# Performance work log

Measured on AMD Instinct MI355X. Metric: run time of the kernel, lower is better.

The kernel has to match this reference:

```python
import jax, jax.numpy as jnp
import numpy as np

D_MODEL = 1024
NUM_HEADS = 16
D_K = D_MODEL // NUM_HEADS


def setup_inputs() -> dict:
    key = jax.random.key(0)
    ks = jax.random.split(key, 12)
    B, S, D = 2, 2048, D_MODEL
    s = 1.0 / np.sqrt(D)
    inp = {
        "Q": jax.random.normal(ks[0], (B, S, D), jnp.float32),
        "K": jax.random.normal(ks[1], (B, S, D), jnp.float32),
        "V": jax.random.normal(ks[2], (B, S, D), jnp.float32),
        "Wq": jax.random.normal(ks[3], (D, D), jnp.float32) * s,
        "bq": jax.random.normal(ks[4], (D,), jnp.float32) * s,
        "Wk": jax.random.normal(ks[5], (D, D), jnp.float32) * s,
        "bk": jax.random.normal(ks[6], (D,), jnp.float32) * s,
        "Wv": jax.random.normal(ks[7], (D, D), jnp.float32) * s,
        "bv": jax.random.normal(ks[8], (D,), jnp.float32) * s,
        "Wo": jax.random.normal(ks[9], (D, D), jnp.float32) * s,
        "bo": jax.random.normal(ks[10], (D,), jnp.float32) * s,
    }
    return inp


def _split_heads(x, B, S):
    # [B, S, D] -> [B, H, S, d_k]
    return x.reshape(B, S, NUM_HEADS, D_K).transpose(0, 2, 1, 3)


def reference(Q, K, V, Wq, bq, Wk, bk, Wv, bv, Wo, bo):
    B, S, D = Q.shape
    # torch nn.Linear: y = x @ W.T + b
    q = _split_heads(Q @ Wq.T + bq, B, S)
    k = _split_heads(K @ Wk.T + bk, B, S)
    v = _split_heads(V @ Wv.T + bv, B, S)
    scale = 1.0 / np.sqrt(D_K).astype(np.float32)
    # [B, H, S, S] attention scores (materialized, as in the original)
    scores = jnp.einsum('bhqd,bhkd->bhqk', q, k) * scale
    probs = jax.nn.softmax(scores, axis=-1)
    out = jnp.einsum('bhqk,bhkd->bhqd', probs, v)
    out = out.transpose(0, 2, 1, 3).reshape(B, S, D)
    return out @ Wo.T + bo
```

## Files before the change

### kernel.cpp

```cpp
#include <hip/hip_runtime.h>
#include <hip/hip_bf16.h>

#define S_LEN   2048
#define NHEADS  16
#define DKH     64
#define DMODEL  1024
#define NBATCH  2

typedef __bf16 bf16x8 __attribute__((ext_vector_type(8)));
typedef __bf16 bf16x4 __attribute__((ext_vector_type(4)));
typedef float  f32x4  __attribute__((ext_vector_type(4)));

typedef __attribute__((address_space(3))) void       lds_void;
typedef const __attribute__((address_space(1))) void glob_void;

__device__ __forceinline__ void glds16(const void* g, void* l) {
    __builtin_amdgcn_global_load_lds((glob_void*)g, (lds_void*)l, 16, 0, 0);
}

struct CvtArgs {
    const float* src[7];
    __bf16*      dst[7];
    int          n[7];
};

__global__ __launch_bounds__(256)
void cvt_all_k(CvtArgs a)
{
    const int t = blockIdx.y;
    const size_t i = ((size_t)blockIdx.x * 256 + threadIdx.x) * 8;
    if ((int)i >= a.n[t]) return;
    const float* s = a.src[t];
    f32x4 lo = *(const f32x4*)(s + i);
    f32x4 hi = *(const f32x4*)(s + i + 4);
    bf16x8 r;
#pragma unroll
    for (int k = 0; k < 4; ++k) { r[k] = (__bf16)lo[k]; r[4 + k] = (__bf16)hi[k]; }
    *(bf16x8*)(a.dst[t] + i) = r;
}

__device__ __forceinline__ void gemm_core(
    const __bf16* __restrict__ A, const __bf16* __restrict__ W,
    int m0, int n0, int K,
    __bf16 (*As)[32], __bf16 (*Ws)[32], f32x4 acc[4][4])
{
    const int tid  = threadIdx.x;
    const int lane = tid & 63;
    const int wv   = tid >> 6;
    const int l15  = lane & 15;
    const int quad = lane >> 4;
    const int wm   = wv >> 1;
    const int wn   = wv & 1;
    const int grow = lane >> 2;
    const int gcol = (lane & 3) * 8;

    const __bf16* ag0 = A + (size_t)(m0 + wv * 32 + grow) * K + gcol;
    const __bf16* ag1 = A + (size_t)(m0 + wv * 32 + 16 + grow) * K + gcol;
    const __bf16* wg0 = W + (size_t)(n0 + wv * 32 + grow) * K + gcol;
    const __bf16* wg1 = W + (size_t)(n0 + wv * 32 + 16 + grow) * K + gcol;
    void* al0 = &As[wv * 32][0];
    void* al1 = &As[wv * 32 + 16][0];
    void* wl0 = &Ws[wv * 32][0];
    void* wl1 = &Ws[wv * 32 + 16][0];

    for (int k0 = 0;;) {
        __syncthreads();
        glds16(ag0 + k0, al0);
        glds16(ag1 + k0, al1);
        glds16(wg0 + k0, wl0);
        glds16(wg1 + k0, wl1);
        __syncthreads();

        bf16x8 af[4], wf[4];
#pragma unroll
        for (int i = 0; i < 4; ++i)
            af[i] = *(const bf16x8*)&As[wm * 64 + i * 16 + l15][quad * 8];
#pragma unroll
        for (int j = 0; j < 4; ++j)
            wf[j] = *(const bf16x8*)&Ws[wn * 64 + j * 16 + l15][quad * 8];
#pragma unroll
        for (int i = 0; i < 4; ++i)
#pragma unroll
            for (int j = 0; j < 4; ++j)
                acc[i][j] = __builtin_amdgcn_mfma_f32_16x16x32_bf16(af[i], wf[j], acc[i][j], 0, 0, 0);

        k0 += 32;
        if (k0 >= K) break;
    }
}

struct GArgs {
    const __bf16* A[3];
    const __bf16* W[3];
    const float*  bias[3];
    __bf16*       out[3];
};

__global__ __launch_bounds__(256)
void gemm_qkv(GArgs g, int z_off)
{
    __shared__ __align__(16) __bf16 As[128][32];
    __shared__ __align__(16) __bf16 Ws[128][32];

    const int fid = blockIdx.x;
    const int z   = (fid >> 8) + z_off;
    const int f8  = fid & 255;
    int m0, n0;
    if (z == 2) { m0 = (f8 & 7) * 128;  n0 = (f8 >> 3) * 128; }
    else        { m0 = (f8 & 31) * 128; n0 = (f8 >> 5) * 128; }

    f32x4 acc[4][4];
#pragma unroll
    for (int i = 0; i < 4; ++i)
#pragma unroll
        for (int j = 0; j < 4; ++j) acc[i][j] = (f32x4){0.f, 0.f, 0.f, 0.f};

    gemm_core(g.A[z], g.W[z], m0, n0, DMODEL, As, Ws, acc);

    const int lane = threadIdx.x & 63;
    const int wv   = threadIdx.x >> 6;
    const int l15  = lane & 15;
    const int quad = lane >> 4;
    const int wm   = wv >> 1;
    const int wn   = wv & 1;
    const float* bias = g.bias[z];
    __bf16* out = g.out[z];
    const float oscale = (z == 0) ? 0.125f * 1.44269504088896f : 1.0f;

#pragma unroll
    for (int j = 0; j < 4; ++j) {
        const int col = n0 + wn * 64 + j * 16 + l15;
        const float bcol = (z == 2) ? 0.f : bias[col];
#pragma unroll
        for (int i = 0; i < 4; ++i) {
#pragma unroll
            for (int r = 0; r < 4; ++r) {
                const int row = m0 + wm * 64 + i * 16 + quad * 4 + r;
                size_t idx;
                float v = acc[i][j][r];
                if (z == 2) {
                    const int h = row >> 6, d = row & (DKH - 1);
                    const int b = col >> 11, s = col & (S_LEN - 1);
                    v += bias[row];
                    idx = ((size_t)(b * NHEADS + h) * DKH + d) * S_LEN + s;
                } else {
                    const int b = row >> 11, s = row & (S_LEN - 1);
                    const int h = col >> 6, d = col & (DKH - 1);
                    v = (v + bcol) * oscale;
                    idx = ((size_t)(b * NHEADS + h) * S_LEN + s) * DKH + d;
                }
                out[idx] = (__bf16)v;
            }
        }
    }
}

__global__ __launch_bounds__(256)
void gemm_out(const __bf16* __restrict__ A, const __bf16* __restrict__ W,
              const float* __restrict__ bias, float* __restrict__ out)
{
    __shared__ __align__(16) __bf16 As[128][32];
    __shared__ __align__(16) __bf16 Ws[128][32];

    const int fid = blockIdx.x;
    const int m0 = (fid & 31) * 128;
    const int n0 = (fid >> 5) * 128;

    f32x4 acc[4][4];
#pragma unroll
    for (int i = 0; i < 4; ++i)
#pragma unroll
        for (int j = 0; j < 4; ++j) acc[i][j] = (f32x4){0.f, 0.f, 0.f, 0.f};

    gemm_core(A, W, m0, n0, DMODEL, As, Ws, acc);

    const int lane = threadIdx.x & 63;
    const int wv   = threadIdx.x >> 6;
    const int l15  = lane & 15;
    const int quad = lane >> 4;
    const int wm   = wv >> 1;
    const int wn   = wv & 1;

#pragma unroll
    for (int j = 0; j < 4; ++j) {
        const int col = n0 + wn * 64 + j * 16 + l15;
        const float bv = bias[col];
#pragma unroll
        for (int i = 0; i < 4; ++i)
#pragma unroll
            for (int r = 0; r < 4; ++r) {
                const int row = m0 + wm * 64 + i * 16 + quad * 4 + r;
                out[(size_t)row * DMODEL + col] = acc[i][j][r] + bv;
            }
    }
}

__global__ __launch_bounds__(256, 2)
void attn_k(const __bf16* __restrict__ Qh, const __bf16* __restrict__ Kh,
            const __bf16* __restrict__ VhT, __bf16* __restrict__ out)
{
    __shared__ __align__(16) __bf16 Ks[128][72];
    __shared__ __align__(16) __bf16 Vs[64][136];

    const int tid  = threadIdx.x;
    const int lane = tid & 63;
    const int wv   = tid >> 6;
    const int l15  = lane & 15;
    const int quad = lane >> 4;

    const int fid = blockIdx.x;
    const int x  = fid & 7;
    const int j  = fid >> 3;
    const int bh = x * 4 + (j & 3);
    const int q0 = (j >> 2) * 128;
    const int b  = bh >> 4;
    const int h  = bh & (NHEADS - 1);

    const __bf16* Q  = Qh  + (size_t)bh * S_LEN * DKH;
    const __bf16* Kp = Kh  + (size_t)bh * S_LEN * DKH;
    const __bf16* Vt = VhT + (size_t)bh * DKH * S_LEN;

    const int qrA = q0 + wv * 32 + l15;
    const int qrB = qrA + 16;
    const bf16x8 qa0 = *(const bf16x8*)(Q + (size_t)qrA * DKH + quad * 8);
    const bf16x8 qa1 = *(const bf16x8*)(Q + (size_t)qrA * DKH + quad * 8 + 32);
    const bf16x8 qb0 = *(const bf16x8*)(Q + (size_t)qrB * DKH + quad * 8);
    const bf16x8 qb1 = *(const bf16x8*)(Q + (size_t)qrB * DKH + quad * 8 + 32);

    const int krow = tid >> 1;
    const int kc0  = (tid & 1) * 32;
    const int vrow = tid >> 2;
    const int vc0  = (tid & 3) * 32;
    const __bf16* kst = Kp + (size_t)krow * DKH   + kc0;
    const __bf16* vst = Vt + (size_t)vrow * S_LEN + vc0;

    f32x4 oA[4], oB[4];
#pragma unroll
    for (int jj = 0; jj < 4; ++jj) {
        oA[jj] = (f32x4){0.f, 0.f, 0.f, 0.f};
        oB[jj] = (f32x4){0.f, 0.f, 0.f, 0.f};
    }
    float laccA = 0.f, laccB = 0.f;

    bf16x8 kr[4], vr[4];
#pragma unroll
    for (int i = 0; i < 4; ++i) kr[i] = *(const bf16x8*)(kst + 8 * i);
#pragma unroll
    for (int i = 0; i < 4; ++i) vr[i] = *(const bf16x8*)(vst + 8 * i);

    for (int kt = 0; kt < S_LEN; kt += 128) {
        __syncthreads();
#pragma unroll
        for (int i = 0; i < 4; ++i) *(bf16x8*)&Ks[krow][kc0 + 8 * i] = kr[i];
#pragma unroll
        for (int i = 0; i < 4; ++i) *(bf16x8*)&Vs[vrow][vc0 + 8 * i] = vr[i];
        __syncthreads();
        if (kt + 128 < S_LEN) {
#pragma unroll
            for (int i = 0; i < 4; ++i)
                kr[i] = *(const bf16x8*)(kst + (size_t)(kt + 128) * DKH + 8 * i);
#pragma unroll
            for (int i = 0; i < 4; ++i)
                vr[i] = *(const bf16x8*)(vst + (kt + 128) + 8 * i);
        }

#pragma unroll
        for (int ht = 0; ht < 2; ++ht) {
            __builtin_amdgcn_s_setprio(1);
            float pA[4][4], pB[4][4];
#pragma unroll
            for (int n = 0; n < 4; ++n) {
                bf16x8 kA = *(const bf16x8*)&Ks[ht * 64 + n * 16 + l15][quad * 8];
                bf16x8 kB = *(const bf16x8*)&Ks[ht * 64 + n * 16 + l15][quad * 8 + 32];
                f32x4 sA = {0.f, 0.f, 0.f, 0.f};
                f32x4 sB = {0.f, 0.f, 0.f, 0.f};
                sA = __builtin_amdgcn_mfma_f32_16x16x32_bf16(kA, qa0, sA, 0, 0, 0);
                sB = __builtin_amdgcn_mfma_f32_16x16x32_bf16(kA, qb0, sB, 0, 0, 0);
                sA = __builtin_amdgcn_mfma_f32_16x16x32_bf16(kB, qa1, sA, 0, 0, 0);
                sB = __builtin_amdgcn_mfma_f32_16x16x32_bf16(kB, qb1, sB, 0, 0, 0);
#pragma unroll
                for (int r = 0; r < 4; ++r) {
                    pA[n][r] = __builtin_amdgcn_exp2f(sA[r]);
                    pB[n][r] = __builtin_amdgcn_exp2f(sB[r]);
                }
            }
#pragma unroll
            for (int n = 0; n < 4; ++n)
#pragma unroll
                for (int r = 0; r < 4; ++r) { laccA += pA[n][r]; laccB += pB[n][r]; }

#pragma unroll
            for (int t = 0; t < 2; ++t) {
                bf16x8 pfA, pfB;
#pragma unroll
                for (int jj = 0; jj < 4; ++jj) {
                    pfA[jj]     = (__bf16)pA[2 * t][jj];
                    pfA[4 + jj] = (__bf16)pA[2 * t + 1][jj];
                    pfB[jj]     = (__bf16)pB[2 * t][jj];
                    pfB[4 + jj] = (__bf16)pB[2 * t + 1][jj];
                }
#pragma unroll
                for (int jt = 0; jt < 4; ++jt) {
                    bf16x4 v0 = *(const bf16x4*)&Vs[jt * 16 + l15][ht * 64 + t * 32 + quad * 4];
                    bf16x4 v1 = *(const bf16x4*)&Vs[jt * 16 + l15][ht * 64 + t * 32 + 16 + quad * 4];
                    bf16x8 vf;
#pragma unroll
                    for (int jj = 0; jj < 4; ++jj) { vf[jj] = v0[jj]; vf[4 + jj] = v1[jj]; }
                    oA[jt] = __builtin_amdgcn_mfma_f32_16x16x32_bf16(vf, pfA, oA[jt], 0, 0, 0);
                    oB[jt] = __builtin_amdgcn_mfma_f32_16x16x32_bf16(vf, pfB, oB[jt], 0, 0, 0);
                }
            }
            __builtin_amdgcn_s_setprio(0);
        }
    }

    laccA += __shfl_xor(laccA, 16);
    laccA += __shfl_xor(laccA, 32);
    laccB += __shfl_xor(laccB, 16);
    laccB += __shfl_xor(laccB, 32);
    const float invA = 1.0f / laccA;
    const float invB = 1.0f / laccB;

    __bf16* opA = out + ((size_t)b * S_LEN + qrA) * DMODEL + h * DKH;
    __bf16* opB = out + ((size_t)b * S_LEN + qrB) * DMODEL + h * DKH;
#pragma unroll
    for (int jt = 0; jt < 4; ++jt) {
        bf16x4 tA, tB;
#pragma unroll
        for (int r = 0; r < 4; ++r) {
            tA[r] = (__bf16)(oA[jt][r] * invA);
            tB[r] = (__bf16)(oB[jt][r] * invB);
        }
        *(bf16x4*)(opA + jt * 16 + quad * 4) = tA;
        *(bf16x4*)(opB + jt * 16 + quad * 4) = tB;
    }
}

extern "C" void kernel_launch(void* const* d_in, const int* in_sizes, int n_in,
                              void* d_out, int out_size, void* d_ws, size_t ws_size,
                              hipStream_t stream) {
    const float* Qi = (const float*)d_in[0];
    const float* Ki = (const float*)d_in[1];
    const float* Vi = (const float*)d_in[2];
    const float* Wq = (const float*)d_in[3];
    const float* bq = (const float*)d_in[4];
    const float* Wk = (const float*)d_in[5];
    const float* bk = (const float*)d_in[6];
    const float* Wv = (const float*)d_in[7];
    const float* bv = (const float*)d_in[8];
    const float* Wo = (const float*)d_in[9];
    const float* bo = (const float*)d_in[10];
    float* out = (float*)d_out;

    const int M = NBATCH * S_LEN;
    const size_t NW = (size_t)DMODEL * DMODEL;
    const size_t NE = (size_t)M * DMODEL;
    const bool big = ws_size >= ((size_t)56 << 20);

    __bf16* w_bf   = (__bf16*)d_ws;
    __bf16* Qin_bf = w_bf + 4 * NW;
    __bf16* Kin_bf = Qin_bf + NE;
    __bf16* Vin_bf = Kin_bf + NE;
    __bf16* q_ws   = Vin_bf + NE;
    __bf16* k_ws   = q_ws + NE;
    __bf16* vT_ws   = big ? (k_ws + NE) : Kin_bf;
    __bf16* attn_ws = Qin_bf;
    __bf16* wq_bf = w_bf, *wk_bf = w_bf + NW, *wv_bf = w_bf + 2 * NW, *wo_bf = w_bf + 3 * NW;

    CvtArgs ca;
    ca.src[0] = Wq; ca.src[1] = Wk; ca.src[2] = Wv; ca.src[3] = Wo;
    ca.src[4] = Qi; ca.src[5] = Ki; ca.src[6] = Vi;
    ca.dst[0] = wq_bf; ca.dst[1] = wk_bf; ca.dst[2] = wv_bf; ca.dst[3] = wo_bf;
    ca.dst[4] = Qin_bf; ca.dst[5] = Kin_bf; ca.dst[6] = Vin_bf;
    for (int t = 0; t < 4; ++t) ca.n[t] = (int)NW;
    for (int t = 4; t < 7; ++t) ca.n[t] = (int)NE;
    cvt_all_k<<<dim3(2048, 7), 256, 0, stream>>>(ca);

    GArgs g;
    g.A[0] = Qin_bf; g.W[0] = wq_bf; g.bias[0] = bq; g.out[0] = q_ws;
    g.A[1] = Kin_bf; g.W[1] = wk_bf; g.bias[1] = bk; g.out[1] = k_ws;
    g.A[2] = wv_bf;  g.W[2] = Vin_bf; g.bias[2] = bv; g.out[2] = vT_ws;
    if (big) {
        gemm_qkv<<<dim3(768), 256, 0, stream>>>(g, 0);
    } else {
        gemm_qkv<<<dim3(512), 256, 0, stream>>>(g, 0);
        gemm_qkv<<<dim3(256), 256, 0, stream>>>(g, 2);
    }

    attn_k<<<dim3(512), dim3(256), 0, stream>>>(q_ws, k_ws, vT_ws, attn_ws);

    gemm_out<<<dim3(256), 256, 0, stream>>>(attn_ws, wo_bf, bo, out);
}
```

Measured before the change: 221.5 us.

## Split attention over key halves with combine pass; widen GEMM K-tile with swizzled LDS

Attention work can now be split across two key-range halves, doubling block count to 1024 (launch bound raised to 4 blocks/SM). Each half writes unnormalized fp32 partial outputs and row sums, and a new combine kernel sums them and normalizes. This only runs when the workspace is large enough. The shared GEMM core now loads a 64-wide K tile per barrier pair with an XOR-swizzled LDS layout, which halves barrier count and avoids bank conflicts. The cost is extra fp32 partial traffic, an extra launch, and twice the GEMM LDS footprint. The split appears to rely on the unnormalized exp sums sharing a fixed max across halves.

Measured after the change: 311.0 us. 1.4x slower.

```diff
diff --git a/kernel.cpp b/kernel.cpp
--- a/kernel.cpp
+++ b/kernel.cpp
@@ -42,7 +42,7 @@
 __device__ __forceinline__ void gemm_core(
     const __bf16* __restrict__ A, const __bf16* __restrict__ W,
     int m0, int n0, int K,
-    __bf16 (*As)[32], __bf16 (*Ws)[32], f32x4 acc[4][4])
+    __bf16 (*As)[64], __bf16 (*Ws)[64], f32x4 acc[4][4])
 {
     const int tid  = threadIdx.x;
     const int lane = tid & 63;
@@ -51,40 +51,48 @@
     const int quad = lane >> 4;
     const int wm   = wv >> 1;
     const int wn   = wv & 1;
-    const int grow = lane >> 2;
-    const int gcol = (lane & 3) * 8;
-
-    const __bf16* ag0 = A + (size_t)(m0 + wv * 32 + grow) * K + gcol;
-    const __bf16* ag1 = A + (size_t)(m0 + wv * 32 + 16 + grow) * K + gcol;
-    const __bf16* wg0 = W + (size_t)(n0 + wv * 32 + grow) * K + gcol;
-    const __bf16* wg1 = W + (size_t)(n0 + wv * 32 + 16 + grow) * K + gcol;
-    void* al0 = &As[wv * 32][0];
-    void* al1 = &As[wv * 32 + 16][0];
-    void* wl0 = &Ws[wv * 32][0];
-    void* wl1 = &Ws[wv * 32 + 16][0];
+    const int srow = lane >> 3;
+    const int scol = ((lane & 7) ^ srow) << 3;
+
+    const __bf16* ag[4]; const __bf16* wg[4];
+    void* al[4]; void* wl[4];
+#pragma unroll
+    for (int i = 0; i < 4; ++i) {
+        const int r = wv * 8 + i * 32 + srow;
+        ag[i] = A + (size_t)(m0 + r) * K + scol;
+        wg[i] = W + (size_t)(n0 + r) * K + scol;
+        al[i] = &As[wv * 8 + i * 32][0];
+        wl[i] = &Ws[wv * 8 + i * 32][0];
+    }
 
     for (int k0 = 0;;) {
         __syncthreads();
-        glds16(ag0 + k0, al0);
-        glds16(ag1 + k0, al1);
-        glds16(wg0 + k0, wl0);
-        glds16(wg1 + k0, wl1);
+#pragma unroll
+        for (int i = 0; i < 4; ++i) { glds16(ag[i] + k0, al[i]); glds16(wg[i] + k0, wl[i]); }
         __syncthreads();
 
-        bf16x8 af[4], wf[4];
-#pragma unroll
-        for (int i = 0; i < 4; ++i)
-            af[i] = *(const bf16x8*)&As[wm * 64 + i * 16 + l15][quad * 8];
-#pragma unroll
-        for (int j = 0; j < 4; ++j)
-            wf[j] = *(const bf16x8*)&Ws[wn * 64 + j * 16 + l15][quad * 8];
-#pragma unroll
-        for (int i = 0; i < 4; ++i)
-#pragma unroll
-            for (int j = 0; j < 4; ++j)
-                acc[i][j] = __builtin_amdgcn_mfma_f32_16x16x32_bf16(af[i], wf[j], acc[i][j], 0, 0, 0);
-
-        k0 += 32;
+#pragma unroll
+        for (int kh = 0; kh < 2; ++kh) {
+            bf16x8 af[4], wf[4];
+#pragma unroll
+            for (int i = 0; i < 4; ++i) {
+                const int row = wm * 64 + i * 16 + l15;
+                af[i] = *(const bf16x8*)((const char*)&As[row][0]
+                        + (((quad << 4) + (kh << 6)) ^ ((row & 7) << 4)));
+            }
+#pragma unroll
+            for (int j = 0; j < 4; ++j) {
+                const int row = wn * 64 + j * 16 + l15;
+                wf[j] = *(const bf16x8*)((const char*)&Ws[row][0]
+                        + (((quad << 4) + (kh << 6)) ^ ((row & 7) << 4)));
+            }
+#pragma unroll
+            for (int i = 0; i < 4; ++i)
+#pragma unroll
+                for (int j = 0; j < 4; ++j)
+                    acc[i][j] = __builtin_amdgcn_mfma_f32_16x16x32_bf16(af[i], wf[j], acc[i][j], 0, 0, 0);
+        }
+        k0 += 64;
         if (k0 >= K) break;
     }
 }
@@ -99,8 +107,8 @@
 __global__ __launch_bounds__(256)
 void gemm_qkv(GArgs g, int z_off)
 {
-    __shared__ __align__(16) __bf16 As[128][32];
-    __shared__ __align__(16) __bf16 Ws[128][32];
+    __shared__ __align__(16) __bf16 As[128][64];
+    __shared__ __align__(16) __bf16 Ws[128][64];
 
     const int fid = blockIdx.x;
     const int z   = (fid >> 8) + z_off;
@@ -159,8 +167,8 @@
 void gemm_out(const __bf16* __restrict__ A, const __bf16* __restrict__ W,
               const float* __restrict__ bias, float* __restrict__ out)
 {
-    __shared__ __align__(16) __bf16 As[128][32];
-    __shared__ __align__(16) __bf16 Ws[128][32];
+    __shared__ __align__(16) __bf16 As[128][64];
+    __shared__ __align__(16) __bf16 Ws[128][64];
 
     const int fid = blockIdx.x;
     const int m0 = (fid & 31) * 128;
@@ -195,9 +203,10 @@
     }
 }
 
-__global__ __launch_bounds__(256, 2)
+__global__ __launch_bounds__(256, 4)
 void attn_k(const __bf16* __restrict__ Qh, const __bf16* __restrict__ Kh,
-            const __bf16* __restrict__ VhT, __bf16* __restrict__ out)
+            const __bf16* __restrict__ VhT, __bf16* __restrict__ out,
+            float* __restrict__ opart, float* __restrict__ lpart, int ksplit)
 {
     __shared__ __align__(16) __bf16 Ks[128][72];
     __shared__ __align__(16) __bf16 Vs[64][136];
@@ -208,11 +217,15 @@
     const int l15  = lane & 15;
     const int quad = lane >> 4;
 
-    const int fid = blockIdx.x;
-    const int x  = fid & 7;
-    const int j  = fid >> 3;
-    const int bh = x * 4 + (j & 3);
-    const int q0 = (j >> 2) * 128;
+    const int fid  = blockIdx.x;
+    const int x    = fid & 7;
+    const int j    = fid >> 3;
+    const int bh   = x * 4 + (j & 3);
+    const int rest = j >> 2;
+    const int q0   = (rest & 15) * 128;
+    const int kh   = rest >> 4;
+    const int klen = S_LEN / ksplit;
+    const int kbeg = kh * klen;
     const int b  = bh >> 4;
     const int h  = bh & (NHEADS - 1);
 
@@ -244,18 +257,18 @@
 
     bf16x8 kr[4], vr[4];
 #pragma unroll
-    for (int i = 0; i < 4; ++i) kr[i] = *(const bf16x8*)(kst + 8 * i);
-#pragma unroll
-    for (int i = 0; i < 4; ++i) vr[i] = *(const bf16x8*)(vst + 8 * i);
-
-    for (int kt = 0; kt < S_LEN; kt += 128) {
+    for (int i = 0; i < 4; ++i) kr[i] = *(const bf16x8*)(kst + (size_t)kbeg * DKH + 8 * i);
+#pragma unroll
+    for (int i = 0; i < 4; ++i) vr[i] = *(const bf16x8*)(vst + kbeg + 8 * i);
+
+    for (int kt = kbeg; kt < kbeg + klen; kt += 128) {
         __syncthreads();
 #pragma unroll
         for (int i = 0; i < 4; ++i) *(bf16x8*)&Ks[krow][kc0 + 8 * i] = kr[i];
 #pragma unroll
         for (int i = 0; i < 4; ++i) *(bf16x8*)&Vs[vrow][vc0 + 8 * i] = vr[i];
         __syncthreads();
-        if (kt + 128 < S_LEN) {
+        if (kt + 128 < kbeg + klen) {
 #pragma unroll
             for (int i = 0; i < 4; ++i)
                 kr[i] = *(const bf16x8*)(kst + (size_t)(kt + 128) * DKH + 8 * i);
@@ -318,22 +331,62 @@
     laccA += __shfl_xor(laccA, 32);
     laccB += __shfl_xor(laccB, 16);
     laccB += __shfl_xor(laccB, 32);
-    const float invA = 1.0f / laccA;
-    const float invB = 1.0f / laccB;
-
-    __bf16* opA = out + ((size_t)b * S_LEN + qrA) * DMODEL + h * DKH;
-    __bf16* opB = out + ((size_t)b * S_LEN + qrB) * DMODEL + h * DKH;
-#pragma unroll
-    for (int jt = 0; jt < 4; ++jt) {
-        bf16x4 tA, tB;
-#pragma unroll
-        for (int r = 0; r < 4; ++r) {
-            tA[r] = (__bf16)(oA[jt][r] * invA);
-            tB[r] = (__bf16)(oB[jt][r] * invB);
-        }
-        *(bf16x4*)(opA + jt * 16 + quad * 4) = tA;
-        *(bf16x4*)(opB + jt * 16 + quad * 4) = tB;
-    }
+
+    if (ksplit == 1) {
+        const float invA = 1.0f / laccA;
+        const float invB = 1.0f / laccB;
+        __bf16* opA = out + ((size_t)b * S_LEN + qrA) * DMODEL + h * DKH;
+        __bf16* opB = out + ((size_t)b * S_LEN + qrB) * DMODEL + h * DKH;
+#pragma unroll
+        for (int jt = 0; jt < 4; ++jt) {
+            bf16x4 tA, tB;
+#pragma unroll
+            for (int r = 0; r < 4; ++r) {
+                tA[r] = (__bf16)(oA[jt][r] * invA);
+                tB[r] = (__bf16)(oB[jt][r] * invB);
+            }
+            *(bf16x4*)(opA + jt * 16 + quad * 4) = tA;
+            *(bf16x4*)(opB + jt * 16 + quad * 4) = tB;
+        }
+    } else {
+        float* pa = opart + ((size_t)(kh * 32 + bh) * S_LEN + qrA) * DKH;
+        float* pb = opart + ((size_t)(kh * 32 + bh) * S_LEN + qrB) * DKH;
+#pragma unroll
+        for (int jt = 0; jt < 4; ++jt) {
+            *(f32x4*)(pa + jt * 16 + quad * 4) = oA[jt];
+            *(f32x4*)(pb + jt * 16 + quad * 4) = oB[jt];
+        }
+        if (quad == 0) {
+            lpart[(size_t)(kh * 32 + bh) * S_LEN + qrA] = laccA;
+            lpart[(size_t)(kh * 32 + bh) * S_LEN + qrB] = laccB;
+        }
+    }
+}
+
+__global__ __launch_bounds__(256)
+void attn_combine(const float* __restrict__ opart, const float* __restrict__ lpart,
+                  __bf16* __restrict__ out)
+{
+    const int t  = blockIdx.x * 256 + threadIdx.x;
+    const int d8 = t & 7;
+    const int s  = (t >> 3) & (S_LEN - 1);
+    const int bh = t >> 14;
+    const size_t half = (size_t)32 * S_LEN * DKH;
+    const size_t base = ((size_t)bh * S_LEN + s) * DKH + d8 * 8;
+    f32x4 a0 = *(const f32x4*)(opart + base);
+    f32x4 a1 = *(const f32x4*)(opart + base + 4);
+    f32x4 b0 = *(const f32x4*)(opart + base + half);
+    f32x4 b1 = *(const f32x4*)(opart + base + half + 4);
+    const float inv = 1.0f / (lpart[(size_t)bh * S_LEN + s]
+                            + lpart[(size_t)(32 + bh) * S_LEN + s]);
+    bf16x8 r;
+#pragma unroll
+    for (int k = 0; k < 4; ++k) {
+        r[k]     = (__bf16)((a0[k] + b0[k]) * inv);
+        r[4 + k] = (__bf16)((a1[k] + b1[k]) * inv);
+    }
+    const int bb = bh >> 4, hh = bh & (NHEADS - 1);
+    *(bf16x8*)(out + ((size_t)bb * S_LEN + s) * DMODEL + hh * DKH + d8 * 8) = r;
 }
 
 extern "C" void kernel_launch(void* const* d_in, const int* in_sizes, int n_in,
@@ -355,16 +408,23 @@
     const int M = NBATCH * S_LEN;
     const size_t NW = (size_t)DMODEL * DMODEL;
     const size_t NE = (size_t)M * DMODEL;
-    const bool big = ws_size >= ((size_t)56 << 20);
+    const size_t MB = (size_t)1 << 20;
 
     __bf16* w_bf   = (__bf16*)d_ws;
-    __bf16* Qin_bf = w_bf + 4 * NW;
+    __bf16* q_ws   = w_bf + 4 * NW;
+    __bf16* k_ws   = q_ws + NE;
+    __bf16* vT_big = k_ws + NE;
+    __bf16* Qin_bf = vT_big + NE;
     __bf16* Kin_bf = Qin_bf + NE;
     __bf16* Vin_bf = Kin_bf + NE;
-    __bf16* q_ws   = Vin_bf + NE;
-    __bf16* k_ws   = q_ws + NE;
-    __bf16* vT_ws   = big ? (k_ws + NE) : Kin_bf;
-    __bf16* attn_ws = Qin_bf;
+    float*  opart  = (float*)Qin_bf;
+    float*  lpart  = (float*)((char*)d_ws + 64 * MB);
+    __bf16* attn2  = (__bf16*)((char*)d_ws + 65 * MB);
+
+    const bool big   = ws_size >= 56 * MB;
+    const int ksplit = (ws_size >= 73 * MB) ? 2 : 1;
+    __bf16* vT_ws   = big ? vT_big : Kin_bf;
+    __bf16* attn_ws = (ksplit == 2) ? attn2 : Qin_bf;
     __bf16* wq_bf = w_bf, *wk_bf = w_bf + NW, *wv_bf = w_bf + 2 * NW, *wo_bf = w_bf + 3 * NW;
 
     CvtArgs ca;
@@ -387,7 +447,10 @@
         gemm_qkv<<<dim3(256), 256, 0, stream>>>(g, 2);
     }
 
-    attn_k<<<dim3(512), dim3(256), 0, stream>>>(q_ws, k_ws, vT_ws, attn_ws);
+    attn_k<<<dim3(512 * ksplit), dim3(256), 0, stream>>>(q_ws, k_ws, vT_ws, attn_ws,
+                                                         opart, lpart, ksplit);
+    if (ksplit == 2)
+        attn_combine<<<dim3(2048), 256, 0, stream>>>(opart, lpart, attn_ws);
 
     gemm_out<<<dim3(256), 256, 0, stream>>>(attn_ws, wo_bf, bo, out);
 }
```

## Replace direct-to-LDS GEMM loads with register-prefetched K=64 padded LDS tiles

Applied to the files above, without the earlier changes.

The GEMM core no longer uses global_load_lds 16-byte copies into an unpadded 32-wide tile. It now loads 64-wide K slices into registers, stores them to padded LDS tiles (row stride 76), and prefetches the next slice into registers while the MFMAs run. This halves the number of barrier pairs per K loop and pads rows to cut LDS bank conflicts on fragment reads. The cost is more LDS, which may lower occupancy, and more VGPRs for the staging registers.

Measured after the change: 350.3 us. 1.58x slower.

```diff
diff --git a/kernel.cpp b/kernel.cpp
--- a/kernel.cpp
+++ b/kernel.cpp
@@ -10,13 +10,6 @@
 typedef __bf16 bf16x8 __attribute__((ext_vector_type(8)));
 typedef __bf16 bf16x4 __attribute__((ext_vector_type(4)));
 typedef float  f32x4  __attribute__((ext_vector_type(4)));
-
-typedef __attribute__((address_space(3))) void       lds_void;
-typedef const __attribute__((address_space(1))) void glob_void;
-
-__device__ __forceinline__ void glds16(const void* g, void* l) {
-    __builtin_amdgcn_global_load_lds((glob_void*)g, (lds_void*)l, 16, 0, 0);
-}
 
 struct CvtArgs {
     const float* src[7];
@@ -42,7 +35,7 @@
 __device__ __forceinline__ void gemm_core(
     const __bf16* __restrict__ A, const __bf16* __restrict__ W,
     int m0, int n0, int K,
-    __bf16 (*As)[32], __bf16 (*Ws)[32], f32x4 acc[4][4])
+    __bf16 (*As)[76], __bf16 (*Ws)[76], f32x4 acc[4][4])
 {
     const int tid  = threadIdx.x;
     const int lane = tid & 63;
@@ -51,41 +44,53 @@
     const int quad = lane >> 4;
     const int wm   = wv >> 1;
     const int wn   = wv & 1;
-    const int grow = lane >> 2;
-    const int gcol = (lane & 3) * 8;
-
-    const __bf16* ag0 = A + (size_t)(m0 + wv * 32 + grow) * K + gcol;
-    const __bf16* ag1 = A + (size_t)(m0 + wv * 32 + 16 + grow) * K + gcol;
-    const __bf16* wg0 = W + (size_t)(n0 + wv * 32 + grow) * K + gcol;
-    const __bf16* wg1 = W + (size_t)(n0 + wv * 32 + 16 + grow) * K + gcol;
-    void* al0 = &As[wv * 32][0];
-    void* al1 = &As[wv * 32 + 16][0];
-    void* wl0 = &Ws[wv * 32][0];
-    void* wl1 = &Ws[wv * 32 + 16][0];
+    const int srow = tid >> 1;
+    const int sc0  = (tid & 1) * 32;
+    const __bf16* ag = A + (size_t)(m0 + srow) * K + sc0;
+    const __bf16* wg = W + (size_t)(n0 + srow) * K + sc0;
+
+    bf16x8 ar[4], wr[4];
+#pragma unroll
+    for (int i = 0; i < 4; ++i) {
+        ar[i] = *(const bf16x8*)(ag + 8 * i);
+        wr[i] = *(const bf16x8*)(wg + 8 * i);
+    }
 
     for (int k0 = 0;;) {
         __syncthreads();
-        glds16(ag0 + k0, al0);
-        glds16(ag1 + k0, al1);
-        glds16(wg0 + k0, wl0);
-        glds16(wg1 + k0, wl1);
+#pragma unroll
+        for (int i = 0; i < 4; ++i) {
+            *(bf16x8*)&As[srow][sc0 + 8 * i] = ar[i];
+            *(bf16x8*)&Ws[srow][sc0 + 8 * i] = wr[i];
+        }
         __syncthreads();
-
-        bf16x8 af[4], wf[4];
-#pragma unroll
-        for (int i = 0; i < 4; ++i)
-            af[i] = *(const bf16x8*)&As[wm * 64 + i * 16 + l15][quad * 8];
-#pragma unroll
-        for (int j = 0; j < 4; ++j)
-            wf[j] = *(const bf16x8*)&Ws[wn * 64 + j * 16 + l15][quad * 8];
-#pragma unroll
-        for (int i = 0; i < 4; ++i)
+        const int nk = k0 + 64;
+        if (nk < K) {
+#pragma unroll
+            for (int i = 0; i < 4; ++i) {
+                ar[i] = *(const bf16x8*)(ag + nk + 8 * i);
+                wr[i] = *(const bf16x8*)(wg + nk + 8 * i);
+            }
+        }
+
+#pragma unroll
+        for (int kh = 0; kh < 2; ++kh) {
+            bf16x8 af[4], wf[4];
+#pragma unroll
+            for (int i = 0; i < 4; ++i)
+                af[i] = *(const bf16x8*)&As[wm * 64 + i * 16 + l15][kh * 32 + quad * 8];
 #pragma unroll
             for (int j = 0; j < 4; ++j)
-                acc[i][j] = __builtin_amdgcn_mfma_f32_16x16x32_bf16(af[i], wf[j], acc[i][j], 0, 0, 0);
-
-        k0 += 32;
-        if (k0 >= K) break;
+                wf[j] = *(const bf16x8*)&Ws[wn * 64 + j * 16 + l15][kh * 32 + quad * 8];
+#pragma unroll
+            for (int i = 0; i < 4; ++i)
+#pragma unroll
+                for (int j = 0; j < 4; ++j)
+                    acc[i][j] = __builtin_amdgcn_mfma_f32_16x16x32_bf16(af[i], wf[j], acc[i][j], 0, 0, 0);
+        }
+
+        if (nk >= K) break;
+        k0 = nk;
     }
 }
 
@@ -99,8 +104,8 @@
 __global__ __launch_bounds__(256)
 void gemm_qkv(GArgs g, int z_off)
 {
-    __shared__ __align__(16) __bf16 As[128][32];
-    __shared__ __align__(16) __bf16 Ws[128][32];
+    __shared__ __align__(16) __bf16 As[128][76];
+    __shared__ __align__(16) __bf16 Ws[128][76];
 
     const int fid = blockIdx.x;
     const int z   = (fid >> 8) + z_off;
@@ -159,8 +164,8 @@
 void gemm_out(const __bf16* __restrict__ A, const __bf16* __restrict__ W,
               const float* __restrict__ bias, float* __restrict__ out)
 {
-    __shared__ __align__(16) __bf16 As[128][32];
-    __shared__ __align__(16) __bf16 Ws[128][32];
+    __shared__ __align__(16) __bf16 As[128][76];
+    __shared__ __align__(16) __bf16 Ws[128][76];
 
     const int fid = blockIdx.x;
     const int m0 = (fid & 31) * 128;
@@ -261,7 +266,7 @@
                 kr[i] = *(const bf16x8*)(kst + (size_t)(kt + 128) * DKH + 8 * i);
 #pragma unroll
             for (int i = 0; i < 4; ++i)
-                vr[i] = *(const bf16x8*)(vst + (kt + 128) + 8 * i);
+                vr[i] = *(const bf16x8*)(vst + kt + 128 + 8 * i);
         }
 
 #pragma unroll
@@ -355,7 +360,6 @@
     const int M = NBATCH * S_LEN;
     const size_t NW = (size_t)DMODEL * DMODEL;
     const size_t NE = (size_t)M * DMODEL;
-    const bool big = ws_size >= ((size_t)56 << 20);
 
     __bf16* w_bf   = (__bf16*)d_ws;
     __bf16* Qin_bf = w_bf + 4 * NW;
@@ -363,6 +367,7 @@
     __bf16* Vin_bf = Kin_bf + NE;
     __bf16* q_ws   = Vin_bf + NE;
     __bf16* k_ws   = q_ws + NE;
+    const bool big = ws_size >= ((size_t)56 << 20);
     __bf16* vT_ws   = big ? (k_ws + NE) : Kin_bf;
     __bf16* attn_ws = Qin_bf;
     __bf16* wq_bf = w_bf, *wk_bf = w_bf + NW, *wv_bf = w_bf + 2 * NW, *wo_bf = w_bf + 3 * NW;
```
